# Optimization experiments

Measured on AMD Instinct MI355X. Metric: run time of the kernel, lower is better.

Reference implementation:

```python
import jax, jax.numpy as jnp
import numpy as np

B, N, H, D, HID = 4, 1024, 16, 72, 1152
ATT = H * D

def setup_inputs() -> dict:
    key = jax.random.key(0)
    ks = jax.random.split(key, 5)
    s = 0.02
    return {
        "x": jax.random.normal(ks[0], (B, N, HID), dtype=jnp.float32),
        "w_qkv": jax.random.normal(ks[1], (HID, 3 * ATT), dtype=jnp.float32) * s,
        "b_qkv": jnp.zeros((3 * ATT,), dtype=jnp.float32),
        "w_out": jax.random.normal(ks[2], (ATT, HID), dtype=jnp.float32) * s,
        "b_out": jnp.zeros((HID,), dtype=jnp.float32),
    }

def reference(x, w_qkv, b_qkv, w_out, b_out):
    # QKV projection: [B,N,3*ATT]
    qkv = x @ w_qkv + b_qkv
    q, k, v = jnp.split(qkv, 3, axis=-1)
    # [B,N,H,D] -> [B,H,N,D]
    q = q.reshape(B, N, H, D).transpose(0, 2, 1, 3)
    k = k.reshape(B, N, H, D).transpose(0, 2, 1, 3)
    v = v.reshape(B, N, H, D).transpose(0, 2, 1, 3)
    scale = D ** -0.5
    att = jnp.einsum("bhqd,bhkd->bhqk", q, k) * scale
    att = jax.nn.softmax(att, axis=-1)
    out = jnp.einsum("bhqk,bhkd->bhqd", att, v)
    out = out.transpose(0, 2, 1, 3).reshape(B, N, ATT)
    return out @ w_out + b_out
```

## Files before the change

### kernel.cpp

```cpp
#include <hip/hip_runtime.h>
#include <cstdint>

#define NB 4
#define NSEQ 1024
#define NH 16
#define HD 72
#define HID 1152
#define QKV3 3456
#define DP 96
#define QSCALE 0.17003713711193175f

typedef __attribute__((ext_vector_type(8))) __bf16 bf16x8;
typedef __attribute__((ext_vector_type(4))) __bf16 bf16x4;
typedef __attribute__((ext_vector_type(4))) float f32x4;

#define AS1 __attribute__((address_space(1)))
#define AS3 __attribute__((address_space(3)))

__device__ __forceinline__ void gl_lds16(const void* g, void* l) {
    __builtin_amdgcn_global_load_lds((const AS1 uint32_t*)g, (AS3 uint32_t*)l, 16, 0, 0);
}

#define RAW_BAR() asm volatile("s_barrier" ::: "memory")

#define XB_OFF     0UL
#define WQKVT_OFF  9437184UL
#define WOUTT_OFF  17694720UL
#define QP_OFF     20643840UL
#define KP_OFF     33226752UL
#define VT_OFF     45809664UL


__global__ void prep_kernel(const float* __restrict__ x, __bf16* __restrict__ xb,
                            const float* __restrict__ w_qkv, __bf16* __restrict__ wqkvT,
                            const float* __restrict__ w_out, __bf16* __restrict__ woutT,
                            __bf16* __restrict__ Qp, __bf16* __restrict__ Kp,
                            __bf16* __restrict__ Vt) {
    __shared__ float t[32][33];
    const int blk = blockIdx.x, tid = threadIdx.x;
    if (blk < 4608) {
        long i = (long)blk * 256 + tid;
        float4 v = ((const float4*)x)[i];
        bf16x4 o = { (__bf16)v.x, (__bf16)v.y, (__bf16)v.z, (__bf16)v.w };
        ((bf16x4*)xb)[i] = o;
    } else if (blk < 9792) {
        const float* in;  __bf16* outp;  int Nc, K, n0, k0;
        if (blk < 8496) {
            int b = blk - 4608; in = w_qkv; outp = wqkvT; Nc = QKV3; K = HID;
            n0 = (b % 108) * 32; k0 = (b / 108) * 32;
        } else {
            int b = blk - 8496; in = w_out; outp = woutT; Nc = HID; K = HID;
            n0 = (b % 36) * 32; k0 = (b / 36) * 32;
        }
        int xx = tid & 31, yy = tid >> 5;
        #pragma unroll
        for (int i = 0; i < 32; i += 8)
            t[yy + i][xx] = in[(long)(k0 + yy + i) * Nc + n0 + xx];
        __syncthreads();
        #pragma unroll
        for (int i = 0; i < 32; i += 8)
            outp[(long)(n0 + yy + i) * K + k0 + xx] = (__bf16)t[xx][yy + i];
    } else {
        int i = (blk - 9792) * 256 + tid;
        uint4 z = make_uint4(0u, 0u, 0u, 0u);
        if (i < 131072) {
            __bf16* base = (i & 65536) ? Kp : Qp;
            int row = i & 65535;
            uint4* p = (uint4*)(base + row * 96 + 72);
            p[0] = z; p[1] = z; p[2] = z;
        } else {
            int j = i - 131072;
            int bh = j / 1536, w = j - bh * 1536;
            *((uint4*)(Vt + (long)bh * 98304 + 73728) + w) = z;
        }
    }
}


template<int MT>
__device__ __forceinline__ void gemm_core(
    const __bf16* __restrict__ A, const __bf16* __restrict__ Bt,
    int lda, int ldb, int ntk, long rowA0, long rowB0,
    char* lds, f32x4 acc[MT][4])
{
    constexpr int BM    = MT * 32;
    constexpr int ATILE = BM * 64;
    constexpr int TILE  = ATILE + 256 * 64;
    constexpr int L     = BM / 128 + 2;

    const int tid  = threadIdx.x;
    const int wave = tid >> 6, lane = tid & 63;
    const int wm = wave >> 2, wn = wave & 3;
    const int lhi = lane >> 4, llo = lane & 15;
    const int srow = tid >> 2;
    const int scol = (tid & 3) * 8;

    auto stage = [&](int kt, int buf) {
        char* base = lds + buf * TILE;
        #pragma unroll
        for (int j = 0; j < BM / 128; ++j) {
            int r  = srow + j * 128;
            int ks = scol ^ ((((unsigned)r >> 1) & 3) << 3);
            gl_lds16(A + (rowA0 + r) * (long)lda + kt * 32 + ks, base + tid * 16 + j * 8192);
        }
        #pragma unroll
        for (int j = 0; j < 2; ++j) {
            int r  = srow + j * 128;
            int ks = scol ^ ((((unsigned)r >> 1) & 3) << 3);
            gl_lds16(Bt + (rowB0 + r) * (long)ldb + kt * 32 + ks,
                     base + ATILE + tid * 16 + j * 8192);
        }
    };

    stage(0, 0);
    stage(1, 1);
    asm volatile("s_waitcnt vmcnt(%0)" :: "n"(L) : "memory");
    RAW_BAR();

    int buf = 0;
    #pragma unroll 1
    for (int t = 0; t < ntk; ++t) {
        char* Ab = lds + buf * TILE;
        char* Bb = Ab + ATILE;
        int nb = buf + 2; if (nb >= 3) nb -= 3;
        if (t + 2 < ntk) stage(t + 2, nb);

        bf16x8 bfr[4];
        #pragma unroll
        for (int nt = 0; nt < 4; ++nt) {
            int R = wn * 64 + nt * 16 + llo;
            int b = (R * 64 + lhi * 16) ^ ((((unsigned)R >> 1) & 3) << 4);
            bfr[nt] = *(const bf16x8*)(Bb + b);
        }
        bf16x8 af[MT / 2];
        #pragma unroll
        for (int mt = 0; mt < MT / 2; ++mt) {
            int R = wm * (BM / 2) + mt * 16 + llo;
            int b = (R * 64 + lhi * 16) ^ ((((unsigned)R >> 1) & 3) << 4);
            af[mt] = *(const bf16x8*)(Ab + b);
        }
        __builtin_amdgcn_s_setprio(1);
        #pragma unroll
        for (int mt = 0; mt < MT / 2; ++mt)
            #pragma unroll
            for (int nt = 0; nt < 4; ++nt)
                acc[mt][nt] = __builtin_amdgcn_mfma_f32_16x16x32_bf16(af[mt], bfr[nt], acc[mt][nt], 0, 0, 0);
        __builtin_amdgcn_s_setprio(0);
        #pragma unroll
        for (int mt = 0; mt < MT / 2; ++mt) {
            int R = wm * (BM / 2) + (MT / 2 + mt) * 16 + llo;
            int b = (R * 64 + lhi * 16) ^ ((((unsigned)R >> 1) & 3) << 4);
            af[mt] = *(const bf16x8*)(Ab + b);
        }
        __builtin_amdgcn_s_setprio(1);
        #pragma unroll
        for (int mt = 0; mt < MT / 2; ++mt)
            #pragma unroll
            for (int nt = 0; nt < 4; ++nt)
                acc[MT / 2 + mt][nt] = __builtin_amdgcn_mfma_f32_16x16x32_bf16(af[mt], bfr[nt], acc[MT / 2 + mt][nt], 0, 0, 0);
        __builtin_amdgcn_s_setprio(0);
        if (t + 2 < ntk)      asm volatile("s_waitcnt vmcnt(%0)" :: "n"(L) : "memory");
        else if (t + 1 < ntk) asm volatile("s_waitcnt vmcnt(0)" ::: "memory");
        RAW_BAR();
        buf = (buf == 2) ? 0 : buf + 1;
    }
}


__global__ __launch_bounds__(512, 4) void gemm_qkv_kernel(
    const __bf16* __restrict__ xb, const __bf16* __restrict__ wqkvT,
    const float* __restrict__ b_qkv,
    __bf16* __restrict__ Qp, __bf16* __restrict__ Kp, __bf16* __restrict__ Vt)
{
    __shared__ char lds[73728];
    f32x4 acc[4][4];
    #pragma unroll
    for (int i = 0; i < 4; ++i)
        #pragma unroll
        for (int j = 0; j < 4; ++j) acc[i][j] = (f32x4){0.f, 0.f, 0.f, 0.f};

    int lin = blockIdx.x;
    int v   = (lin & 7) * 56 + (lin >> 3);
    int bx  = v / 14, by = v - bx * 14;
    long rowA0 = (long)bx * 128, rowB0 = (long)by * 256;

    gemm_core<4>(xb, wqkvT, HID, HID, HID / 32, rowA0, rowB0, lds, acc);

    const int wave = threadIdx.x >> 6, lane = threadIdx.x & 63;
    const int wm = wave >> 2, wn = wave & 3, lhi = lane >> 4, llo = lane & 15;

    #pragma unroll
    for (int nt = 0; nt < 4; ++nt) {
        int n = (int)rowB0 + wn * 64 + nt * 16 + llo;
        if (n >= QKV3) continue;
        int sec = n / HID;
        int nn  = n - sec * HID;
        int h   = nn / HD;
        int d   = nn - h * HD;
        float bias = b_qkv[n];
        if (sec == 2) {
            #pragma unroll
            for (int mt = 0; mt < 4; ++mt) {
                int m0 = (int)rowA0 + wm * 64 + mt * 16 + lhi * 4;
                int bb = m0 >> 10, nq0 = m0 & 1023;
                bf16x4 pk = { (__bf16)(acc[mt][nt][0] + bias), (__bf16)(acc[mt][nt][1] + bias),
                              (__bf16)(acc[mt][nt][2] + bias), (__bf16)(acc[mt][nt][3] + bias) };
                *(bf16x4*)(Vt + ((long)(bb * NH + h) * DP + d) * NSEQ + nq0) = pk;
            }
        } else {
            __bf16* dst = (sec == 0) ? Qp : Kp;
            float scl = (sec == 0) ? QSCALE : 1.0f;
            #pragma unroll
            for (int mt = 0; mt < 4; ++mt) {
                #pragma unroll
                for (int r = 0; r < 4; ++r) {
                    int m = (int)rowA0 + wm * 64 + mt * 16 + lhi * 4 + r;
                    int bb = m >> 10, nq = m & 1023;
                    long bhn = (long)(bb * NH + h) * NSEQ + nq;
                    dst[bhn * DP + d] = (__bf16)((acc[mt][nt][r] + bias) * scl);
                }
            }
        }
    }
}


__global__ __launch_bounds__(512, 4) void flash_kernel(
    const __bf16* __restrict__ Qp, const __bf16* __restrict__ Kp,
    const __bf16* __restrict__ Vt, __bf16* __restrict__ atto)
{
    __shared__ char lds[73728];
    const int tid  = threadIdx.x;
    const int wave = tid >> 6, lane = tid & 63;
    const int lhi = lane >> 4, llo = lane & 15;

    int lin = blockIdx.x;
    int v   = ((lin & 7) << 6) + (lin >> 3);
    const int qx = v & 7;
    const int bh = v >> 3;

    const __bf16* Qb  = Qp + (long)bh * NSEQ * DP;
    const char*   KbB = (const char*)(Kp + (long)bh * NSEQ * DP);
    const char*   VbB = (const char*)(Vt + (long)bh * DP * NSEQ);

    char* P = lds + 57344 + wave * 2048;
    const int q0 = qx * 128 + wave * 16;

    auto stageK = [&](int kt, int kbuf) {
        #pragma unroll
        for (int j = 0; j < 2; ++j) {
            int bk  = wave * 2 + j;
            int key = bk * 4 + (lane >> 4);
            int c   = (lane & 15) * 16;
            gl_lds16(KbB + ((long)(kt * 64 + key)) * 192 + (c ^ ((key & 15) << 4)),
                     lds + kbuf * 16384 + bk * 1024);
        }
    };
    auto stageV = [&](int kt, int vb) {
        int dv = wave * 8 + (lane >> 3);
        int c  = (lane & 7) * 16;
        gl_lds16(VbB + (long)dv * 2048 + kt * 128 + (c ^ ((dv & 7) << 4)),
                 lds + 32768 + vb * 12288 + wave * 1024);
        if (wave < 4) {
            int dv2 = 64 + wave * 8 + (lane >> 3);
            gl_lds16(VbB + (long)dv2 * 2048 + kt * 128 + (c ^ ((dv2 & 7) << 4)),
                     lds + 32768 + vb * 12288 + 8192 + wave * 1024);
        }
    };

    bf16x8 aq[3];
    #pragma unroll
    for (int dc = 0; dc < 3; ++dc)
        aq[dc] = *(const bf16x8*)(Qb + (long)(q0 + llo) * DP + dc * 32 + lhi * 8);

    float mr = -3.0e38f, lr = 0.f;
    f32x4 acc[5];
    #pragma unroll
    for (int t = 0; t < 5; ++t) acc[t] = (f32x4){0.f, 0.f, 0.f, 0.f};

    stageK(0, 0);
    stageV(0, 0);
    asm volatile("s_waitcnt vmcnt(0)" ::: "memory");
    RAW_BAR();

    #pragma unroll 1
    for (int kb = 0; kb < 16; ++kb) {
        const int buf = kb & 1;
        if (kb < 15) {
            stageK(kb + 1, buf ^ 1);
            stageV(kb + 1, buf ^ 1);
        }

        f32x4 s[4];
        __builtin_amdgcn_s_setprio(1);
        #pragma unroll
        for (int ct = 0; ct < 4; ++ct) {
            f32x4 z = (f32x4){0.f, 0.f, 0.f, 0.f};
            #pragma unroll
            for (int dc = 0; dc < 3; ++dc) {
                bf16x8 kf = *(const bf16x8*)(lds + buf * 16384 +
                    (((ct * 16 + llo) * 256 + dc * 64 + lhi * 16) ^ ((llo & 15) << 4)));
                z = __builtin_amdgcn_mfma_f32_16x16x32_bf16(kf, aq[dc], z, 0, 0, 0);
            }
            s[ct] = z;
        }
        __builtin_amdgcn_s_setprio(0);

        float m0 = fmaxf(fmaxf(s[0][0], s[0][1]), fmaxf(s[0][2], s[0][3]));
        float m1 = fmaxf(fmaxf(s[1][0], s[1][1]), fmaxf(s[1][2], s[1][3]));
        float m2 = fmaxf(fmaxf(s[2][0], s[2][1]), fmaxf(s[2][2], s[2][3]));
        float m3 = fmaxf(fmaxf(s[3][0], s[3][1]), fmaxf(s[3][2], s[3][3]));
        float mx = fmaxf(fmaxf(m0, m1), fmaxf(m2, m3));
        mx = fmaxf(mx, __shfl_xor(mx, 16, 64));
        mx = fmaxf(mx, __shfl_xor(mx, 32, 64));
        if (!__all(mx <= mr + 8.0f)) {
            float mn = fmaxf(mr, mx);
            float al = exp2f(mr - mn);
            mr = mn;
            lr *= al;
            #pragma unroll
            for (int t = 0; t < 5; ++t)
                #pragma unroll
                for (int r = 0; r < 4; ++r) acc[t][r] *= al;
        }
        float p[4][4]; float sm = 0.f;
        #pragma unroll
        for (int ct = 0; ct < 4; ++ct)
            #pragma unroll
            for (int r = 0; r < 4; ++r) { p[ct][r] = exp2f(s[ct][r] - mr); sm += p[ct][r]; }
        sm += __shfl_xor(sm, 16, 64);
        sm += __shfl_xor(sm, 32, 64);
        lr += sm;
        #pragma unroll
        for (int ct = 0; ct < 4; ++ct) {
            bf16x4 pk = { (__bf16)p[ct][0], (__bf16)p[ct][1], (__bf16)p[ct][2], (__bf16)p[ct][3] };
            *(bf16x4*)(P + ((llo * 128 + ct * 32 + lhi * 8) ^ ((llo & 7) << 4))) = pk;
        }
        asm volatile("s_waitcnt lgkmcnt(0)" ::: "memory");

        __builtin_amdgcn_s_setprio(1);
        #pragma unroll
        for (int nc = 0; nc < 2; ++nc) {
            bf16x8 pP = *(const bf16x8*)(P + ((llo * 128 + nc * 64 + lhi * 16) ^ ((llo & 7) << 4)));
            #pragma unroll
            for (int t = 0; t < 5; ++t) {
                bf16x8 bv = *(const bf16x8*)(lds + 32768 + buf * 12288 +
                    (((t * 16 + llo) * 128 + nc * 64 + lhi * 16) ^ ((llo & 7) << 4)));
                acc[t] = __builtin_amdgcn_mfma_f32_16x16x32_bf16(bv, pP, acc[t], 0, 0, 0);
            }
        }
        __builtin_amdgcn_s_setprio(0);

        if (kb < 15) asm volatile("s_waitcnt vmcnt(0)" ::: "memory");
        RAW_BAR();
    }

    const float linv = 1.f / lr;
    const int b = bh >> 4, h = bh & 15;
    const int q = q0 + llo;
    __bf16* outP = atto + (long)(b * NSEQ + q) * HID + h * HD;
    #pragma unroll
    for (int t = 0; t < 5; ++t) {
        int d0 = t * 16 + lhi * 4;
        if (d0 < HD) {
            bf16x4 o = { (__bf16)(acc[t][0] * linv), (__bf16)(acc[t][1] * linv),
                         (__bf16)(acc[t][2] * linv), (__bf16)(acc[t][3] * linv) };
            *(bf16x4*)(outP + d0) = o;
        }
    }
}


__global__ __launch_bounds__(512, 4) void gemm_out_kernel(
    const __bf16* __restrict__ atto, const __bf16* __restrict__ woutT,
    const float* __restrict__ b_out, float* __restrict__ out)
{
    __shared__ char lds[73728];
    f32x4 acc[4][4];
    #pragma unroll
    for (int i = 0; i < 4; ++i)
        #pragma unroll
        for (int j = 0; j < 4; ++j) acc[i][j] = (f32x4){0.f, 0.f, 0.f, 0.f};

    int lin = blockIdx.x;
    int v   = (lin & 7) * 20 + (lin >> 3);
    int bx  = v / 5, by = v - bx * 5;
    long rowA0 = (long)bx * 128, rowB0 = (long)by * 256;

    gemm_core<4>(atto, woutT, HID, HID, HID / 32, rowA0, rowB0, lds, acc);

    const int wave = threadIdx.x >> 6, lane = threadIdx.x & 63;
    const int wm = wave >> 2, wn = wave & 3, lhi = lane >> 4, llo = lane & 15;

    #pragma unroll
    for (int nt = 0; nt < 4; ++nt) {
        int n = (int)rowB0 + wn * 64 + nt * 16 + llo;
        if (n >= HID) continue;
        float bias = b_out[n];
        #pragma unroll
        for (int mt = 0; mt < 4; ++mt) {
            #pragma unroll
            for (int r = 0; r < 4; ++r) {
                int m = (int)rowA0 + wm * 64 + mt * 16 + lhi * 4 + r;
                out[(long)m * HID + n] = acc[mt][nt][r] + bias;
            }
        }
    }
}


extern "C" void kernel_launch(void* const* d_in, const int* in_sizes, int n_in,
                              void* d_out, int out_size, void* d_ws, size_t ws_size,
                              hipStream_t stream) {
    const float* x      = (const float*)d_in[0];
    const float* w_qkv  = (const float*)d_in[1];
    const float* b_qkv  = (const float*)d_in[2];
    const float* w_out  = (const float*)d_in[3];
    const float* b_out  = (const float*)d_in[4];
    float* out = (float*)d_out;
    char* ws = (char*)d_ws;

    __bf16* xb    = (__bf16*)(ws + XB_OFF);
    __bf16* atto  = (__bf16*)(ws + XB_OFF);
    __bf16* wqkvT = (__bf16*)(ws + WQKVT_OFF);
    __bf16* woutT = (__bf16*)(ws + WOUTT_OFF);
    __bf16* Qp    = (__bf16*)(ws + QP_OFF);
    __bf16* Kp    = (__bf16*)(ws + KP_OFF);
    __bf16* Vt    = (__bf16*)(ws + VT_OFF);

    prep_kernel<<<10688, 256, 0, stream>>>(x, xb, w_qkv, wqkvT, w_out, woutT, Qp, Kp, Vt);
    gemm_qkv_kernel<<<448, 512, 0, stream>>>(xb, wqkvT, b_qkv, Qp, Kp, Vt);
    flash_kernel<<<512, 512, 0, stream>>>(Qp, Kp, Vt, atto);
    gemm_out_kernel<<<160, 512, 0, stream>>>(atto, woutT, b_out, out);
}
```

Before: 127.2 us.

## Shrink flash attention tiles to 64 queries and 32-key blocks

Reorganizes the flash attention kernel so each block uses 4 waves over 64 queries (1024 blocks instead of 512) and streams 32-key tiles instead of 64, which cuts LDS use from 72KB to 32KB. It also reworks the K/V staging and swizzled LDS addressing to fit the new tile shapes. The aim is higher occupancy and better spread across CUs. The cost is twice as many loop iterations with a barrier each, and K/V reloaded by twice as many blocks.

```diff
diff --git a/kernel.cpp b/kernel.cpp
--- a/kernel.cpp
+++ b/kernel.cpp
@@ -225,46 +225,47 @@
 }
 
 
-__global__ __launch_bounds__(512, 4) void flash_kernel(
+__global__ __launch_bounds__(256, 5) void flash_kernel(
     const __bf16* __restrict__ Qp, const __bf16* __restrict__ Kp,
     const __bf16* __restrict__ Vt, __bf16* __restrict__ atto)
 {
-    __shared__ char lds[73728];
+    __shared__ char lds[32768];
     const int tid  = threadIdx.x;
     const int wave = tid >> 6, lane = tid & 63;
     const int lhi = lane >> 4, llo = lane & 15;
 
     int lin = blockIdx.x;
-    int v   = ((lin & 7) << 6) + (lin >> 3);
-    const int qx = v & 7;
-    const int bh = v >> 3;
+    int v   = ((lin & 7) << 7) + (lin >> 3);
+    const int qx = v & 15;
+    const int bh = v >> 4;
 
     const __bf16* Qb  = Qp + (long)bh * NSEQ * DP;
     const char*   KbB = (const char*)(Kp + (long)bh * NSEQ * DP);
     const char*   VbB = (const char*)(Vt + (long)bh * DP * NSEQ);
 
-    char* P = lds + 57344 + wave * 2048;
-    const int q0 = qx * 128 + wave * 16;
+    char* P = lds + 28672 + wave * 1024;
+    const int q0 = qx * 64 + wave * 16;
 
     auto stageK = [&](int kt, int kbuf) {
         #pragma unroll
         for (int j = 0; j < 2; ++j) {
-            int bk  = wave * 2 + j;
-            int key = bk * 4 + (lane >> 4);
-            int c   = (lane & 15) * 16;
-            gl_lds16(KbB + ((long)(kt * 64 + key)) * 192 + (c ^ ((key & 15) << 4)),
-                     lds + kbuf * 16384 + bk * 1024);
+            int c = tid + j * 256;
+            int r = c >> 4, p = c & 15;
+            gl_lds16(KbB + (long)(kt * 32 + r) * 192 + ((p ^ (r & 15)) << 4),
+                     lds + kbuf * 8192 + c * 16);
         }
     };
     auto stageV = [&](int kt, int vb) {
-        int dv = wave * 8 + (lane >> 3);
-        int c  = (lane & 7) * 16;
-        gl_lds16(VbB + (long)dv * 2048 + kt * 128 + (c ^ ((dv & 7) << 4)),
-                 lds + 32768 + vb * 12288 + wave * 1024);
-        if (wave < 4) {
-            int dv2 = 64 + wave * 8 + (lane >> 3);
-            gl_lds16(VbB + (long)dv2 * 2048 + kt * 128 + (c ^ ((dv2 & 7) << 4)),
-                     lds + 32768 + vb * 12288 + 8192 + wave * 1024);
+        #pragma unroll
+        for (int j = 0; j < 2; ++j) {
+            int c = tid + j * 256;
+            if (c < 384) {
+                int r2 = c >> 3, p = c & 7;
+                int f  = (p << 4) ^ ((r2 & 7) << 4);
+                int d  = 2 * r2 + (f >> 6);
+                gl_lds16(VbB + (long)d * 2048 + kt * 64 + (f & 63),
+                         lds + 16384 + vb * 6144 + c * 16);
+            }
         }
     };
 
@@ -284,22 +285,22 @@
     RAW_BAR();
 
     #pragma unroll 1
-    for (int kb = 0; kb < 16; ++kb) {
+    for (int kb = 0; kb < 32; ++kb) {
         const int buf = kb & 1;
-        if (kb < 15) {
+        if (kb < 31) {
             stageK(kb + 1, buf ^ 1);
             stageV(kb + 1, buf ^ 1);
         }
 
-        f32x4 s[4];
+        f32x4 s[2];
         __builtin_amdgcn_s_setprio(1);
         #pragma unroll
-        for (int ct = 0; ct < 4; ++ct) {
+        for (int ct = 0; ct < 2; ++ct) {
             f32x4 z = (f32x4){0.f, 0.f, 0.f, 0.f};
             #pragma unroll
             for (int dc = 0; dc < 3; ++dc) {
-                bf16x8 kf = *(const bf16x8*)(lds + buf * 16384 +
-                    (((ct * 16 + llo) * 256 + dc * 64 + lhi * 16) ^ ((llo & 15) << 4)));
+                bf16x8 kf = *(const bf16x8*)(lds + buf * 8192 +
+                    (ct * 16 + llo) * 256 + ((dc * 64 + lhi * 16) ^ (llo << 4)));
                 z = __builtin_amdgcn_mfma_f32_16x16x32_bf16(kf, aq[dc], z, 0, 0, 0);
             }
             s[ct] = z;
@@ -308,9 +309,7 @@
 
         float m0 = fmaxf(fmaxf(s[0][0], s[0][1]), fmaxf(s[0][2], s[0][3]));
         float m1 = fmaxf(fmaxf(s[1][0], s[1][1]), fmaxf(s[1][2], s[1][3]));
-        float m2 = fmaxf(fmaxf(s[2][0], s[2][1]), fmaxf(s[2][2], s[2][3]));
-        float m3 = fmaxf(fmaxf(s[3][0], s[3][1]), fmaxf(s[3][2], s[3][3]));
-        float mx = fmaxf(fmaxf(m0, m1), fmaxf(m2, m3));
+        float mx = fmaxf(m0, m1);
         mx = fmaxf(mx, __shfl_xor(mx, 16, 64));
         mx = fmaxf(mx, __shfl_xor(mx, 32, 64));
         if (!__all(mx <= mr + 8.0f)) {
@@ -323,35 +322,34 @@
                 #pragma unroll
                 for (int r = 0; r < 4; ++r) acc[t][r] *= al;
         }
-        float p[4][4]; float sm = 0.f;
-        #pragma unroll
-        for (int ct = 0; ct < 4; ++ct)
+        float p[2][4]; float sm = 0.f;
+        #pragma unroll
+        for (int ct = 0; ct < 2; ++ct)
             #pragma unroll
             for (int r = 0; r < 4; ++r) { p[ct][r] = exp2f(s[ct][r] - mr); sm += p[ct][r]; }
         sm += __shfl_xor(sm, 16, 64);
         sm += __shfl_xor(sm, 32, 64);
         lr += sm;
         #pragma unroll
-        for (int ct = 0; ct < 4; ++ct) {
+        for (int ct = 0; ct < 2; ++ct) {
             bf16x4 pk = { (__bf16)p[ct][0], (__bf16)p[ct][1], (__bf16)p[ct][2], (__bf16)p[ct][3] };
-            *(bf16x4*)(P + ((llo * 128 + ct * 32 + lhi * 8) ^ ((llo & 7) << 4))) = pk;
+            *(bf16x4*)(P + llo * 64 + ((ct * 32 + lhi * 8) ^ ((llo & 3) << 4))) = pk;
         }
         asm volatile("s_waitcnt lgkmcnt(0)" ::: "memory");
 
         __builtin_amdgcn_s_setprio(1);
-        #pragma unroll
-        for (int nc = 0; nc < 2; ++nc) {
-            bf16x8 pP = *(const bf16x8*)(P + ((llo * 128 + nc * 64 + lhi * 16) ^ ((llo & 7) << 4)));
-            #pragma unroll
-            for (int t = 0; t < 5; ++t) {
-                bf16x8 bv = *(const bf16x8*)(lds + 32768 + buf * 12288 +
-                    (((t * 16 + llo) * 128 + nc * 64 + lhi * 16) ^ ((llo & 7) << 4)));
-                acc[t] = __builtin_amdgcn_mfma_f32_16x16x32_bf16(bv, pP, acc[t], 0, 0, 0);
-            }
+        bf16x8 pP = *(const bf16x8*)(P + llo * 64 + ((lhi * 16) ^ ((llo & 3) << 4)));
+        #pragma unroll
+        for (int t = 0; t < 5; ++t) {
+            int r2 = t * 8 + (llo >> 1);
+            int o  = (llo & 1) * 64 + lhi * 16;
+            bf16x8 bv = *(const bf16x8*)(lds + 16384 + buf * 6144 +
+                r2 * 128 + (o ^ ((r2 & 7) << 4)));
+            acc[t] = __builtin_amdgcn_mfma_f32_16x16x32_bf16(bv, pP, acc[t], 0, 0, 0);
         }
         __builtin_amdgcn_s_setprio(0);
 
-        if (kb < 15) asm volatile("s_waitcnt vmcnt(0)" ::: "memory");
+        if (kb < 31) asm volatile("s_waitcnt vmcnt(0)" ::: "memory");
         RAW_BAR();
     }
 
@@ -430,6 +428,6 @@
 
     prep_kernel<<<10688, 256, 0, stream>>>(x, xb, w_qkv, wqkvT, w_out, woutT, Qp, Kp, Vt);
     gemm_qkv_kernel<<<448, 512, 0, stream>>>(xb, wqkvT, b_qkv, Qp, Kp, Vt);
-    flash_kernel<<<512, 512, 0, stream>>>(Qp, Kp, Vt, atto);
+    flash_kernel<<<1024, 256, 0, stream>>>(Qp, Kp, Vt, atto);
     gemm_out_kernel<<<160, 512, 0, stream>>>(atto, woutT, b_out, out);
 }
```

New measurement: 134.2 us. 1.06x slower.
